# Kernel tuning notes

Measured on AMD Instinct MI355X. Metric: run time of the kernel, lower is better.

## Reference

```python
import jax, jax.numpy as jnp
import numpy as np

PI = float(np.pi)

def setup_inputs() -> dict:
    key = jax.random.key(0)
    k1, k2 = jax.random.split(key)
    inp = jax.random.normal(k1, (16, 4096, 512), dtype=jnp.float32)
    lengths = jax.random.randint(k2, (16,), 0, 4096, dtype=jnp.int32)
    return {"inp": inp, "lengths": lengths}

def reference(inp, lengths):
    B, S, D = inp.shape
    pos = jnp.arange(S, dtype=jnp.float32)                      # [S]
    lens = lengths.astype(jnp.float32)[:, None]                  # [B,1]
    safe_len = jnp.maximum(lens, 1.0)
    # cos(x / len * pi) for x < len, else 0 (matches torch.zeros init)
    pe = jnp.where(pos[None, :] < lens,
                   jnp.cos(pos[None, :] / safe_len * PI),
                   0.0)                                          # [B,S]
    pe = pe.astype(inp.dtype)
    # original intent: concatenate positional channel along feature dim
    return jnp.concatenate([inp, pe[:, :, None]], axis=2)        # [B,S,D+1]
```

## Files before the change

### kernel.cpp

```cpp
#include <hip/hip_runtime.h>
#include <hip/hip_bf16.h>
#include <math.h>


#define PB 16
#define PS 4096
#define PD 512
#define PI_F 3.14159265358979323846f

__global__ __launch_bounds__(256) void sinpe_kernel(
    const float* __restrict__ inp,
    const int* __restrict__ lengths,
    float* __restrict__ out)
{
    const int row = blockIdx.x;
    const int s   = row & (PS - 1);
    const int b   = row >> 12;

    const float* __restrict__ in_row  = inp + (size_t)row * PD;
    float* __restrict__       out_row = out + (size_t)row * (PD + 1);

    const int t = threadIdx.x;

    out_row[t]       = in_row[t];
    out_row[t + 256] = in_row[t + 256];

    if (t == 0) {
        const int len = lengths[b];
        float pe = 0.0f;
        if (s < len) {
            const float fl = fmaxf((float)len, 1.0f);
            pe = cosf(((float)s / fl) * PI_F);
        }
        out_row[PD] = pe;
    }
}

extern "C" void kernel_launch(void* const* d_in, const int* in_sizes, int n_in,
                              void* d_out, int out_size, void* d_ws, size_t ws_size,
                              hipStream_t stream)
{
    const float* inp     = (const float*)d_in[0];
    const int*   lengths = (const int*)d_in[1];
    float*       out     = (float*)d_out;

    const int n_rows = PB * PS;
    sinpe_kernel<<<n_rows, 256, 0, stream>>>(inp, lengths, out);
}
```

Measured before the change: 218.8 us.

## Write output as aligned float4 over 4-row groups with grid-stride loop

Rows have 513 floats, so output rows are misaligned. The kernel now groups four rows (2052 floats, 513 float4s) so every output store is an aligned 16-byte float4 write. Each thread gathers its four values from the input with scalar loads and computes the PE value inline where a row boundary falls. A grid-stride loop with fewer blocks replaces one block per row. The cost is scalar unaligned-pattern input loads and an integer divide by 513 per element.

```diff
diff --git a/kernel.cpp b/kernel.cpp
--- a/kernel.cpp
+++ b/kernel.cpp
@@ -6,33 +6,48 @@
 #define PB 16
 #define PS 4096
 #define PD 512
+#define NROWS   (PB * PS)
+#define NGROUPS (NROWS / 4)
+#define NF4     (NGROUPS * 513)
 #define PI_F 3.14159265358979323846f
 
 __global__ __launch_bounds__(256) void sinpe_kernel(
     const float* __restrict__ inp,
     const int* __restrict__ lengths,
-    float* __restrict__ out)
+    float4* __restrict__ out)
 {
-    const int row = blockIdx.x;
-    const int s   = row & (PS - 1);
-    const int b   = row >> 12;
+    const int stride = gridDim.x * blockDim.x;
+    for (int fidx = blockIdx.x * blockDim.x + threadIdx.x; fidx < NF4;
+         fidx += stride)
+    {
+        const unsigned g = (unsigned)fidx / 513u;
+        const unsigned j = (unsigned)fidx - g * 513u;
+        const int d0  = 4 * (int)j;
+        const int gin = (int)g * 2048;
 
-    const float* __restrict__ in_row  = inp + (size_t)row * PD;
-    float* __restrict__       out_row = out + (size_t)row * (PD + 1);
-
-    const int t = threadIdx.x;
-
-    out_row[t]       = in_row[t];
-    out_row[t + 256] = in_row[t + 256];
-
-    if (t == 0) {
-        const int len = lengths[b];
-        float pe = 0.0f;
-        if (s < len) {
-            const float fl = fmaxf((float)len, 1.0f);
-            pe = cosf(((float)s / fl) * PI_F);
+        float vals[4];
+        #pragma unroll
+        for (int k = 0; k < 4; ++k) {
+            const int d = d0 + k;
+            const int r = (d >= 1539) ? 3 : (d >= 1026) ? 2 : (d >= 513) ? 1 : 0;
+            const int col = d - 513 * r;
+            if (col < PD) {
+                vals[k] = inp[gin + d - r];
+            } else {
+                const int row = (int)g * 4 + r;
+                const int s   = row & (PS - 1);
+                const int b   = row >> 12;
+                const int len = lengths[b];
+                float pe = 0.0f;
+                if (s < len) {
+                    pe = cosf(((float)s / fmaxf((float)len, 1.0f)) * PI_F);
+                }
+                vals[k] = pe;
+            }
         }
-        out_row[PD] = pe;
+        float4 v;
+        v.x = vals[0]; v.y = vals[1]; v.z = vals[2]; v.w = vals[3];
+        out[fidx] = v;
     }
 }
 
@@ -42,8 +57,8 @@
 {
     const float* inp     = (const float*)d_in[0];
     const int*   lengths = (const int*)d_in[1];
-    float*       out     = (float*)d_out;
+    float4*      out     = (float4*)d_out;
 
-    const int n_rows = PB * PS;
-    sinpe_kernel<<<n_rows, 256, 0, stream>>>(inp, lengths, out);
+    const int blocks = NF4 / (256 * 4);
+    sinpe_kernel<<<blocks, 256, 0, stream>>>(inp, lengths, out);
 }
```

Measured after the change: 233.9 us. 1.07x slower.

## Stage 8 rows through LDS to emit fully aligned float4 stores

Applied to the files above, without the earlier changes.

Each block now handles 8 rows. It loads them with float4 reads, scatters them into shared memory in the padded D+1 output layout, inserts the positional values, then writes the contiguous output chunk back with aligned float4 stores. The old kernel issued misaligned scalar stores because each output row stride is 513 floats. The change aims for wide, coalesced global stores on this memory-bound copy, at the cost of an LDS round trip, bank conflicts on the scalar LDS writes and a block barrier.

```diff
diff --git a/kernel.cpp b/kernel.cpp
--- a/kernel.cpp
+++ b/kernel.cpp
@@ -6,33 +6,58 @@
 #define PB 16
 #define PS 4096
 #define PD 512
+#define ROWS_PER_BLOCK 8
+#define IN_DW   (ROWS_PER_BLOCK * PD)
+#define OUT_DW  (ROWS_PER_BLOCK * (PD + 1))
+#define IN_F4   (IN_DW / 4)
+#define OUT_F4  (OUT_DW / 4)
+#define NBLOCKS ((PB * PS) / ROWS_PER_BLOCK)
 #define PI_F 3.14159265358979323846f
 
 __global__ __launch_bounds__(256) void sinpe_kernel(
-    const float* __restrict__ inp,
+    const float4* __restrict__ in4,
     const int* __restrict__ lengths,
-    float* __restrict__ out)
+    float4* __restrict__ out4)
 {
-    const int row = blockIdx.x;
-    const int s   = row & (PS - 1);
-    const int b   = row >> 12;
+    __shared__ __align__(16) float lds[OUT_DW];
 
-    const float* __restrict__ in_row  = inp + (size_t)row * PD;
-    float* __restrict__       out_row = out + (size_t)row * (PD + 1);
+    const int blk = blockIdx.x;
+    const int t   = threadIdx.x;
 
-    const int t = threadIdx.x;
+    const float4* __restrict__ in_base = in4 + (size_t)blk * IN_F4;
+    #pragma unroll
+    for (int j = 0; j < 4; ++j) {
+        const int f = j * 256 + t;
+        const float4 v = in_base[f];
+        const int D = f * 4;
+        const int r = D >> 9;
+        const int c = D & (PD - 1);
+        float* p = &lds[r * (PD + 1) + c];
+        p[0] = v.x; p[1] = v.y; p[2] = v.z; p[3] = v.w;
+    }
 
-    out_row[t]       = in_row[t];
-    out_row[t + 256] = in_row[t + 256];
-
-    if (t == 0) {
+    if (t < ROWS_PER_BLOCK) {
+        const int row = blk * ROWS_PER_BLOCK + t;
+        const int s   = row & (PS - 1);
+        const int b   = row >> 12;
         const int len = lengths[b];
         float pe = 0.0f;
         if (s < len) {
-            const float fl = fmaxf((float)len, 1.0f);
-            pe = cosf(((float)s / fl) * PI_F);
+            pe = cosf(((float)s / fmaxf((float)len, 1.0f)) * PI_F);
         }
-        out_row[PD] = pe;
+        lds[t * (PD + 1) + PD] = pe;
+    }
+
+    __syncthreads();
+
+    float4* __restrict__ out_base = out4 + (size_t)blk * OUT_F4;
+    const float4* __restrict__ lds4 = (const float4*)lds;
+    #pragma unroll
+    for (int j = 0; j < 5; ++j) {
+        const int o = j * 256 + t;
+        if (o < OUT_F4) {
+            out_base[o] = lds4[o];
+        }
     }
 }
 
@@ -40,10 +65,9 @@
                               void* d_out, int out_size, void* d_ws, size_t ws_size,
                               hipStream_t stream)
 {
-    const float* inp     = (const float*)d_in[0];
-    const int*   lengths = (const int*)d_in[1];
-    float*       out     = (float*)d_out;
+    const float4* in4     = (const float4*)d_in[0];
+    const int*    lengths = (const int*)d_in[1];
+    float4*       out4    = (float4*)d_out;
 
-    const int n_rows = PB * PS;
-    sinpe_kernel<<<n_rows, 256, 0, stream>>>(inp, lengths, out);
+    sinpe_kernel<<<NBLOCKS, 256, 0, stream>>>(in4, lengths, out4);
 }
```

After: 231.6 us. +5.9%, slower.
